# Kernel optimization log

Measured on AMD Instinct MI355X. Metric: run time of the kernel, lower is better.

The kernel has to match this reference:

```python
import jax, jax.numpy as jnp
import numpy as np

N, D_IN, HID, N_CLS, E = 100000, 256, 128, 41, 1600000


def setup_inputs() -> dict:
    key = jax.random.key(0)
    ks = jax.random.split(key, 8)
    x = jax.random.normal(ks[0], (N, D_IN), dtype=jnp.float32)
    edge_index = jax.random.randint(ks[1], (2, E), 0, N, dtype=jnp.int64)
    s = 1.0 / np.sqrt(D_IN)
    W1 = jax.random.uniform(ks[2], (D_IN, HID), jnp.float32, -s, s)
    b1 = jnp.zeros((HID,), jnp.float32)
    s2 = 1.0 / np.sqrt(HID)
    W2 = jax.random.uniform(ks[3], (HID, HID), jnp.float32, -s2, s2)
    b2 = jnp.zeros((HID,), jnp.float32)
    lin_w = jax.random.uniform(ks[4], (HID, N_CLS), jnp.float32, -s2, s2)
    lin_b = jnp.zeros((N_CLS,), jnp.float32)
    return {"x": x, "edge_index": edge_index, "W1": W1, "b1": b1,
            "W2": W2, "b2": b2, "lin_w": lin_w, "lin_b": lin_b}


def _gcn_conv(h, src, dst, norm, W, b, n):
    # h: [N, F_in]; transform then gather-scale-scatter (PyG GCNConv order)
    h = h @ W                                   # [N, F_out]
    msg = h[src] * norm[:, None]                # [E+N, F_out]
    return jax.ops.segment_sum(msg, dst, num_segments=n) + b


def reference(x, edge_index, W1, b1, W2, b2, lin_w, lin_b):
    n = x.shape[0]
    loops = jnp.arange(n, dtype=edge_index.dtype)
    src = jnp.concatenate([edge_index[0], loops])  # add self-loops
    dst = jnp.concatenate([edge_index[1], loops])
    # symmetric normalization D^-1/2 (A+I) D^-1/2
    deg = jax.ops.segment_sum(jnp.ones_like(dst, dtype=x.dtype), dst, num_segments=n)
    dis = jnp.where(deg > 0, jax.lax.rsqrt(jnp.maximum(deg, 1.0)), 0.0)
    norm = dis[src] * dis[dst]                   # [E+N]

    x1 = jax.nn.relu(_gcn_conv(x, src, dst, norm, W1, b1, n))   # dropout is identity in eval
    x2 = jax.nn.relu(_gcn_conv(x1, src, dst, norm, W2, b2, n))
    out = (x1 + x2) @ lin_w + lin_b
    return jax.nn.log_softmax(out, axis=1)
```

## Files before the change

kernel.cpp:

```cpp
#include <hip/hip_runtime.h>
#include <math.h>


#define NPAD (1 << 17)
#define CHUNK 1024

typedef __attribute__((ext_vector_type(8))) short short8;
typedef __attribute__((ext_vector_type(4))) float f32x4;

__device__ inline unsigned short f2bf(float f) {
    unsigned u = __builtin_bit_cast(unsigned, f);
    return (unsigned short)((u + 0x7fffu + ((u >> 16) & 1u)) >> 16);
}
__device__ inline float bflo(unsigned u) { return __builtin_bit_cast(float, u << 16); }
__device__ inline float bfhi(unsigned u) { return __builtin_bit_cast(float, u & 0xffff0000u); }


__global__ void mega1(const int* __restrict__ dst, int* __restrict__ cnt, int E, int histB,
                      const float* __restrict__ W1, unsigned short* __restrict__ Wt1,
                      const float* __restrict__ W2, unsigned short* __restrict__ Wt2) {
    int b = blockIdx.x;
    if (b < histB) {
        int e = b * 256 + threadIdx.x;
        if (e < E) atomicAdd(&cnt[dst[e]], 1);
    } else {
        int i = (b - histB) * 256 + threadIdx.x;
        if (i < 256 * 128) {
            int k = i >> 7, nn = i & 127;
            Wt1[nn * 256 + k] = f2bf(W1[i]);
        } else {
            int j = i - 256 * 128;
            if (j < 128 * 128) {
                int k = j >> 7, nn = j & 127;
                Wt2[nn * 128 + k] = f2bf(W2[j]);
            }
        }
    }
}

__global__ void scan_partial(const int* __restrict__ cnt, int* __restrict__ partial, int n) {
    __shared__ int sdata[4];
    int b = blockIdx.x, t = threadIdx.x;
    int base = b * CHUNK;
    int sum = 0;
    for (int i = t; i < CHUNK; i += 256) {
        int idx = base + i;
        if (idx < n) sum += cnt[idx];
    }
#pragma unroll
    for (int off = 32; off > 0; off >>= 1) sum += __shfl_down(sum, off, 64);
    if ((t & 63) == 0) sdata[t >> 6] = sum;
    __syncthreads();
    if (t == 0) partial[b] = sdata[0] + sdata[1] + sdata[2] + sdata[3];
}

__global__ void scan_small(int* partial, int nblk) {
    __shared__ int sm[128];
    int t = threadIdx.x;
    int v = (t < nblk) ? partial[t] : 0;
    int x = v;
    sm[t] = x;
    __syncthreads();
    for (int off = 1; off < 128; off <<= 1) {
        int y = (t >= off) ? sm[t - off] : 0;
        __syncthreads();
        x += y;
        sm[t] = x;
        __syncthreads();
    }
    if (t < nblk) partial[t] = x - v;
}

__global__ void scan_final(const int* __restrict__ cnt, const int* __restrict__ partial,
                           int* __restrict__ offs, int* __restrict__ cursor,
                           float* __restrict__ dis, int n) {
    __shared__ int wsum[4];
    int b = blockIdx.x, t = threadIdx.x;
    int lane = t & 63, w = t >> 6;
    int base = b * CHUNK + t * 4;
    int v[4];
#pragma unroll
    for (int j = 0; j < 4; j++) v[j] = (base + j < n) ? cnt[base + j] : 0;
    int s4 = v[0] + v[1] + v[2] + v[3];
    int inc = s4;
#pragma unroll
    for (int off = 1; off < 64; off <<= 1) {
        int x = __shfl_up(inc, off, 64);
        if (lane >= off) inc += x;
    }
    if (lane == 63) wsum[w] = inc;
    __syncthreads();
    int woff = 0;
    for (int i = 0; i < 4; i++) if (i < w) woff += wsum[i];
    int pos = partial[b] + woff + (inc - s4);
#pragma unroll
    for (int j = 0; j < 4; j++) {
        int idx = base + j;
        if (idx < n) {
            offs[idx] = pos;
            cursor[idx] = pos;
            dis[idx] = rsqrtf((float)(v[j] + 1));
            pos += v[j];
        }
    }
}

__global__ void permute_all(const int* __restrict__ src, const int* __restrict__ dst,
                            const float* __restrict__ dis,
                            int* __restrict__ cursor, int2* __restrict__ eadj, int E) {
    int e = blockIdx.x * 256 + threadIdx.x;
    if (e < E) {
        int d = dst[e];
        int s = src[e];
        int pos = atomicAdd(&cursor[d], 1);
        eadj[pos] = make_int2(s, __float_as_int(dis[s] * dis[d]));
    }
}

template<bool ABF16>
__device__ void gemm_body(int bid, const void* __restrict__ Ap,
                          const unsigned short* __restrict__ Wt,
                          unsigned short* __restrict__ Hb,
                          int n, int K, unsigned short* bs) {
    const int tid = threadIdx.x;
    const int wave = tid >> 6, lane = tid & 63;
    const int quad = lane >> 4, mrow = lane & 15;
    const int arow_g = bid * 64 + wave * 16 + mrow;
    const int arow = arow_g < n ? arow_g : n - 1;

    f32x4 acc[8];
#pragma unroll
    for (int t = 0; t < 8; t++) acc[t] = (f32x4){0.f, 0.f, 0.f, 0.f};

    const float* Af = (const float*)Ap;
    const unsigned short* Ab = (const unsigned short*)Ap;

    for (int kc = 0; kc < K; kc += 128) {
        __syncthreads();
        for (int i = tid; i < 2048; i += 256) {
            int row = i >> 4, c8 = i & 15;
            *(short8*)&bs[row * 136 + c8 * 8] = *(const short8*)&Wt[row * K + kc + c8 * 8];
        }
        __syncthreads();
#pragma unroll
        for (int kt = 0; kt < 128; kt += 32) {
            union { short8 v; unsigned short u[8]; } A;
            if (ABF16) {
                A.v = *(const short8*)&Ab[(size_t)arow * K + kc + kt + quad * 8];
            } else {
                const float* ap = &Af[(size_t)arow * K + kc + kt + quad * 8];
                float4 p0 = *(const float4*)ap;
                float4 p1 = *(const float4*)(ap + 4);
                A.u[0] = f2bf(p0.x); A.u[1] = f2bf(p0.y);
                A.u[2] = f2bf(p0.z); A.u[3] = f2bf(p0.w);
                A.u[4] = f2bf(p1.x); A.u[5] = f2bf(p1.y);
                A.u[6] = f2bf(p1.z); A.u[7] = f2bf(p1.w);
            }
#pragma unroll
            for (int nt = 0; nt < 8; nt++) {
                short8 B = *(const short8*)&bs[(nt * 16 + mrow) * 136 + kt + quad * 8];
                acc[nt] = __builtin_amdgcn_mfma_f32_16x16x32_bf16(A.v, B, acc[nt], 0, 0, 0);
            }
        }
    }
    const int drow0 = bid * 64 + wave * 16 + quad * 4;
#pragma unroll
    for (int r = 0; r < 4; r++) {
        int dr = drow0 + r;
        if (dr < n) {
#pragma unroll
            for (int nt = 0; nt < 8; nt++)
                Hb[(size_t)dr * 128 + nt * 16 + mrow] = f2bf(acc[nt][r]);
        }
    }
}

__global__ __launch_bounds__(256) void gemm1_k(const float* __restrict__ x,
                                               const unsigned short* __restrict__ Wt1,
                                               unsigned short* __restrict__ Hb, int n) {
    __shared__ unsigned short bs[128 * 136];
    gemm_body<false>(blockIdx.x, x, Wt1, Hb, n, 256, bs);
}

__global__ __launch_bounds__(256) void gemm2_k(const unsigned short* __restrict__ X1b,
                                               const unsigned short* __restrict__ Wt2,
                                               unsigned short* __restrict__ Hb, int n) {
    __shared__ unsigned short bs[128 * 136];
    gemm_body<true>(blockIdx.x, X1b, Wt2, Hb, n, 128, bs);
}

__global__ __launch_bounds__(256) void gather_h(const unsigned short* __restrict__ Hb,
                                                const int2* __restrict__ eadj,
                                                const int* __restrict__ offs,
                                                const int* __restrict__ cnt,
                                                const float* __restrict__ dis,
                                                const float* __restrict__ bias,
                                                unsigned short* __restrict__ outb,
                                                int n) {
    const int b = blockIdx.x;
    const int xcd = b & 7;
    const int half = xcd >> 2;
    const int nb = ((b >> 3) << 2) | (xcd & 3);
    const int w = threadIdx.x >> 6, lane = threadIdx.x & 63;
    const int grp = lane >> 3, fl = lane & 7;
    const int node = nb * 4 + w;
    const int nd = node < n ? node : n - 1;
    const int st = offs[nd], c = cnt[nd];
    const unsigned short* Hfl = Hb + half * 64 + fl * 8;

    float acc[8];
#pragma unroll
    for (int k = 0; k < 8; k++) acc[k] = 0.f;

    const int2* ep = eadj + st;
    for (int kk = 0; kk < c; kk += 64) {
        int li = kk + lane;
        int2 me = ep[li < c ? li : c - 1];
        float mw = li < c ? __int_as_float(me.y) : 0.f;
        int cend = (c - kk) < 64 ? (c - kk) : 64;

        int   s0 = __shfl(me.x, grp, 64);
        float w0 = __shfl(mw,  grp, 64);
        int   s1 = __shfl(me.x, 8 + grp, 64);
        float w1 = __shfl(mw,  8 + grp, 64);
        uint4 r0 = *(const uint4*)(Hfl + (size_t)s0 * 128);
        uint4 r1 = *(const uint4*)(Hfl + (size_t)s1 * 128);

        for (int j = 0; j < cend; j += 16) {
            int jn = (j + 16 < cend) ? j + 16 : j;
            int   sn0 = __shfl(me.x, jn + grp, 64);
            float wn0 = __shfl(mw,  jn + grp, 64);
            int   sn1 = __shfl(me.x, jn + 8 + grp, 64);
            float wn1 = __shfl(mw,  jn + 8 + grp, 64);
            uint4 rn0 = *(const uint4*)(Hfl + (size_t)sn0 * 128);
            uint4 rn1 = *(const uint4*)(Hfl + (size_t)sn1 * 128);
            acc[0] = fmaf(bflo(r0.x), w0, acc[0]); acc[1] = fmaf(bfhi(r0.x), w0, acc[1]);
            acc[2] = fmaf(bflo(r0.y), w0, acc[2]); acc[3] = fmaf(bfhi(r0.y), w0, acc[3]);
            acc[4] = fmaf(bflo(r0.z), w0, acc[4]); acc[5] = fmaf(bfhi(r0.z), w0, acc[5]);
            acc[6] = fmaf(bflo(r0.w), w0, acc[6]); acc[7] = fmaf(bfhi(r0.w), w0, acc[7]);
            acc[0] = fmaf(bflo(r1.x), w1, acc[0]); acc[1] = fmaf(bfhi(r1.x), w1, acc[1]);
            acc[2] = fmaf(bflo(r1.y), w1, acc[2]); acc[3] = fmaf(bfhi(r1.y), w1, acc[3]);
            acc[4] = fmaf(bflo(r1.z), w1, acc[4]); acc[5] = fmaf(bfhi(r1.z), w1, acc[5]);
            acc[6] = fmaf(bflo(r1.w), w1, acc[6]); acc[7] = fmaf(bfhi(r1.w), w1, acc[7]);
            r0 = rn0; r1 = rn1; w0 = wn0; w1 = wn1;
        }
    }
#pragma unroll
    for (int k = 0; k < 8; k++) {
        acc[k] += __shfl_xor(acc[k], 8, 64);
        acc[k] += __shfl_xor(acc[k], 16, 64);
        acc[k] += __shfl_xor(acc[k], 32, 64);
    }
    float dd = dis[nd], sn = dd * dd;
    uint4 rs = *(const uint4*)(Hfl + (size_t)nd * 128);
    float4 bb0 = ((const float4*)bias)[half * 16 + fl * 2];
    float4 bb1 = ((const float4*)bias)[half * 16 + fl * 2 + 1];
    acc[0] = fmaf(bflo(rs.x), sn, acc[0]) + bb0.x;
    acc[1] = fmaf(bfhi(rs.x), sn, acc[1]) + bb0.y;
    acc[2] = fmaf(bflo(rs.y), sn, acc[2]) + bb0.z;
    acc[3] = fmaf(bfhi(rs.y), sn, acc[3]) + bb0.w;
    acc[4] = fmaf(bflo(rs.z), sn, acc[4]) + bb1.x;
    acc[5] = fmaf(bfhi(rs.z), sn, acc[5]) + bb1.y;
    acc[6] = fmaf(bflo(rs.w), sn, acc[6]) + bb1.z;
    acc[7] = fmaf(bfhi(rs.w), sn, acc[7]) + bb1.w;
#pragma unroll
    for (int k = 0; k < 8; k++) acc[k] = acc[k] > 0.f ? acc[k] : 0.f;

    if (node < n && grp == 0) {
        uint4 pk;
        pk.x = ((unsigned)f2bf(acc[1]) << 16) | (unsigned)f2bf(acc[0]);
        pk.y = ((unsigned)f2bf(acc[3]) << 16) | (unsigned)f2bf(acc[2]);
        pk.z = ((unsigned)f2bf(acc[5]) << 16) | (unsigned)f2bf(acc[4]);
        pk.w = ((unsigned)f2bf(acc[7]) << 16) | (unsigned)f2bf(acc[6]);
        *(uint4*)(outb + (size_t)node * 128 + half * 64 + fl * 8) = pk;
    }
}

__global__ __launch_bounds__(256) void head_k(const unsigned short* __restrict__ x1b,
                                              const unsigned short* __restrict__ x2b,
                                              const float* __restrict__ lw,
                                              const float* __restrict__ lb,
                                              float* __restrict__ out, int n, int nblk) {
    __shared__ float lws[128 * 41];
    __shared__ float s[4][128];
    const int tid = threadIdx.x;
    const int w = tid >> 6, lane = tid & 63;
    for (int i = tid; i < 128 * 41; i += 256) lws[i] = lw[i];
    __syncthreads();
    const float lbv = (lane < 41) ? lb[lane] : 0.f;

    for (int blk = blockIdx.x; blk * 4 < n; blk += nblk) {
        const int node = blk * 4 + w;
        const int nd = node < n ? node : n - 1;
        unsigned u1 = *(const unsigned*)(x1b + (size_t)nd * 128 + lane * 2);
        unsigned u2 = *(const unsigned*)(x2b + (size_t)nd * 128 + lane * 2);
        s[w][lane * 2]     = bflo(u1) + bflo(u2);
        s[w][lane * 2 + 1] = bfhi(u1) + bfhi(u2);
        const bool act = (node < n) && (lane < 41);
        float v0 = 0.f, v1 = 0.f, v2 = 0.f, v3 = 0.f;
        if (act) {
#pragma unroll 8
            for (int f = 0; f < 32; f++) {
                v0 = fmaf(s[w][f],      lws[f * 41 + lane],        v0);
                v1 = fmaf(s[w][f + 32], lws[(f + 32) * 41 + lane], v1);
                v2 = fmaf(s[w][f + 64], lws[(f + 64) * 41 + lane], v2);
                v3 = fmaf(s[w][f + 96], lws[(f + 96) * 41 + lane], v3);
            }
        }
        float val = (v0 + v1) + (v2 + v3) + lbv;
        float m = act ? val : -INFINITY;
#pragma unroll
        for (int off = 32; off > 0; off >>= 1) m = fmaxf(m, __shfl_xor(m, off, 64));
        float e = act ? expf(val - m) : 0.f;
#pragma unroll
        for (int off = 32; off > 0; off >>= 1) e += __shfl_xor(e, off, 64);
        if (act) out[(size_t)node * 41 + lane] = val - m - logf(e);
    }
}

extern "C" void kernel_launch(void* const* d_in, const int* in_sizes, int n_in,
                              void* d_out, int out_size, void* d_ws, size_t ws_size,
                              hipStream_t stream) {
    const float* x  = (const float*)d_in[0];
    const int*   ei = (const int*)d_in[1];
    const float* W1 = (const float*)d_in[2];
    const float* b1 = (const float*)d_in[3];
    const float* W2 = (const float*)d_in[4];
    const float* b2 = (const float*)d_in[5];
    const float* lw = (const float*)d_in[6];
    const float* lb = (const float*)d_in[7];
    float* out = (float*)d_out;

    const int n = in_sizes[0] / 256;
    const int E = in_sizes[1] / 2;
    const int* src = ei;
    const int* dst = ei + E;

    int*   cnt     = (int*)d_ws;
    int*   offs    = cnt + NPAD;
    int*   cursor  = offs + NPAD;
    int*   partial = cursor + NPAD;
    float* dis     = (float*)(partial + 1024);
    size_t Epad    = ((size_t)E + 255) & ~(size_t)255;
    int2*  eadj    = (int2*)(dis + NPAD);
    unsigned short* Wt1 = (unsigned short*)(eadj + Epad);
    unsigned short* Wt2 = Wt1 + 256 * 128;
    unsigned short* Hb  = Wt2 + 128 * 128;
    unsigned short* X1b = Hb + (size_t)n * 128;
    unsigned short* X2b = X1b + (size_t)n * 128;

    const int nscan = (n + CHUNK - 1) / CHUNK;
    const int histB = (E + 255) / 256;
    const int wcastB = (256 * 128 + 128 * 128 + 255) / 256;
    const int gemmB = (n + 63) / 64;
    const int NB = (n + 3) / 4;
    const int gathB = 8 * ((NB + 3) / 4);
    const int headB = 1536;

    hipMemsetAsync(cnt, 0, (size_t)n * sizeof(int), stream);

    mega1<<<histB + wcastB, 256, 0, stream>>>(dst, cnt, E, histB, W1, Wt1, W2, Wt2);
    scan_partial<<<nscan, 256, 0, stream>>>(cnt, partial, n);
    scan_small<<<1, 128, 0, stream>>>(partial, nscan);
    scan_final<<<nscan, 256, 0, stream>>>(cnt, partial, offs, cursor, dis, n);
    permute_all<<<histB, 256, 0, stream>>>(src, dst, dis, cursor, eadj, E);

    gemm1_k<<<gemmB, 256, 0, stream>>>(x, Wt1, Hb, n);
    gather_h<<<gathB, 256, 0, stream>>>(Hb, eadj, offs, cnt, dis, b1, X1b, n);

    gemm2_k<<<gemmB, 256, 0, stream>>>(X1b, Wt2, Hb, n);
    gather_h<<<gathB, 256, 0, stream>>>(Hb, eadj, offs, cnt, dis, b2, X2b, n);

    head_k<<<headB, 256, 0, stream>>>(X1b, X2b, lw, lb, out, n, headB);
}
```

Before: 640.7 us.

## Compute classifier head with split-bf16 MFMA instead of scalar FMA loop

```diff
diff --git a/kernel.cpp b/kernel.cpp
--- a/kernel.cpp
+++ b/kernel.cpp
@@ -12,13 +12,18 @@
     unsigned u = __builtin_bit_cast(unsigned, f);
     return (unsigned short)((u + 0x7fffu + ((u >> 16) & 1u)) >> 16);
 }
+__device__ inline float bf2f(unsigned short h) {
+    return __builtin_bit_cast(float, (unsigned)h << 16);
+}
 __device__ inline float bflo(unsigned u) { return __builtin_bit_cast(float, u << 16); }
 __device__ inline float bfhi(unsigned u) { return __builtin_bit_cast(float, u & 0xffff0000u); }
 
 
 __global__ void mega1(const int* __restrict__ dst, int* __restrict__ cnt, int E, int histB,
                       const float* __restrict__ W1, unsigned short* __restrict__ Wt1,
-                      const float* __restrict__ W2, unsigned short* __restrict__ Wt2) {
+                      const float* __restrict__ W2, unsigned short* __restrict__ Wt2,
+                      const float* __restrict__ lw, unsigned short* __restrict__ lwt_hi,
+                      unsigned short* __restrict__ lwt_lo) {
     int b = blockIdx.x;
     if (b < histB) {
         int e = b * 256 + threadIdx.x;
@@ -28,11 +33,18 @@
         if (i < 256 * 128) {
             int k = i >> 7, nn = i & 127;
             Wt1[nn * 256 + k] = f2bf(W1[i]);
+        } else if (i < 256 * 128 + 128 * 128) {
+            int j = i - 256 * 128;
+            int k = j >> 7, nn = j & 127;
+            Wt2[nn * 128 + k] = f2bf(W2[j]);
         } else {
-            int j = i - 256 * 128;
-            if (j < 128 * 128) {
-                int k = j >> 7, nn = j & 127;
-                Wt2[nn * 128 + k] = f2bf(W2[j]);
+            int j = i - (256 * 128 + 128 * 128);
+            if (j < 48 * 128) {
+                int c = j >> 7, k = j & 127;
+                float wv = (c < 41) ? lw[k * 41 + c] : 0.f;
+                unsigned short hi = f2bf(wv);
+                lwt_hi[c * 128 + k] = hi;
+                lwt_lo[c * 128 + k] = f2bf(wv - bf2f(hi));
             }
         }
     }
@@ -278,43 +290,84 @@
 
 __global__ __launch_bounds__(256) void head_k(const unsigned short* __restrict__ x1b,
                                               const unsigned short* __restrict__ x2b,
-                                              const float* __restrict__ lw,
+                                              const unsigned short* __restrict__ lwt_hi,
+                                              const unsigned short* __restrict__ lwt_lo,
                                               const float* __restrict__ lb,
-                                              float* __restrict__ out, int n, int nblk) {
-    __shared__ float lws[128 * 41];
-    __shared__ float s[4][128];
+                                              float* __restrict__ out, int n) {
+    __shared__ unsigned short Ah[64][136];
+    __shared__ unsigned short Al[64][136];
+    __shared__ unsigned short Bh[48][136];
+    __shared__ unsigned short Bl[48][136];
     const int tid = threadIdx.x;
-    const int w = tid >> 6, lane = tid & 63;
-    for (int i = tid; i < 128 * 41; i += 256) lws[i] = lw[i];
+    const int wave = tid >> 6, lane = tid & 63;
+    const int quad = lane >> 4, mrow = lane & 15;
+    const int base = blockIdx.x * 64;
+
+    for (int i = tid; i < 1024; i += 256) {
+        int row = i >> 4, oct = i & 15;
+        int node = base + row; int nd = node < n ? node : n - 1;
+        uint4 u1 = *(const uint4*)(x1b + (size_t)nd * 128 + oct * 8);
+        uint4 u2 = *(const uint4*)(x2b + (size_t)nd * 128 + oct * 8);
+        unsigned uu1[4] = {u1.x, u1.y, u1.z, u1.w};
+        unsigned uu2[4] = {u2.x, u2.y, u2.z, u2.w};
+        union { short8 v; unsigned short u[8]; } H, L;
+#pragma unroll
+        for (int q = 0; q < 4; q++) {
+            float vl = bflo(uu1[q]) + bflo(uu2[q]);
+            float vh = bfhi(uu1[q]) + bfhi(uu2[q]);
+            unsigned short hl = f2bf(vl), hh = f2bf(vh);
+            H.u[q * 2]     = hl;  L.u[q * 2]     = f2bf(vl - bf2f(hl));
+            H.u[q * 2 + 1] = hh;  L.u[q * 2 + 1] = f2bf(vh - bf2f(hh));
+        }
+        *(short8*)&Ah[row][oct * 8] = H.v;
+        *(short8*)&Al[row][oct * 8] = L.v;
+    }
+    for (int i = tid; i < 768; i += 256) {
+        int row = i >> 4, oct = i & 15;
+        *(short8*)&Bh[row][oct * 8] = *(const short8*)&lwt_hi[row * 128 + oct * 8];
+        *(short8*)&Bl[row][oct * 8] = *(const short8*)&lwt_lo[row * 128 + oct * 8];
+    }
     __syncthreads();
-    const float lbv = (lane < 41) ? lb[lane] : 0.f;
-
-    for (int blk = blockIdx.x; blk * 4 < n; blk += nblk) {
-        const int node = blk * 4 + w;
-        const int nd = node < n ? node : n - 1;
-        unsigned u1 = *(const unsigned*)(x1b + (size_t)nd * 128 + lane * 2);
-        unsigned u2 = *(const unsigned*)(x2b + (size_t)nd * 128 + lane * 2);
-        s[w][lane * 2]     = bflo(u1) + bflo(u2);
-        s[w][lane * 2 + 1] = bfhi(u1) + bfhi(u2);
-        const bool act = (node < n) && (lane < 41);
-        float v0 = 0.f, v1 = 0.f, v2 = 0.f, v3 = 0.f;
-        if (act) {
-#pragma unroll 8
-            for (int f = 0; f < 32; f++) {
-                v0 = fmaf(s[w][f],      lws[f * 41 + lane],        v0);
-                v1 = fmaf(s[w][f + 32], lws[(f + 32) * 41 + lane], v1);
-                v2 = fmaf(s[w][f + 64], lws[(f + 64) * 41 + lane], v2);
-                v3 = fmaf(s[w][f + 96], lws[(f + 96) * 41 + lane], v3);
-            }
-        }
-        float val = (v0 + v1) + (v2 + v3) + lbv;
-        float m = act ? val : -INFINITY;
-#pragma unroll
-        for (int off = 32; off > 0; off >>= 1) m = fmaxf(m, __shfl_xor(m, off, 64));
-        float e = act ? expf(val - m) : 0.f;
-#pragma unroll
-        for (int off = 32; off > 0; off >>= 1) e += __shfl_xor(e, off, 64);
-        if (act) out[(size_t)node * 41 + lane] = val - m - logf(e);
+
+    f32x4 acc[3];
+#pragma unroll
+    for (int nt = 0; nt < 3; nt++) acc[nt] = (f32x4){0.f, 0.f, 0.f, 0.f};
+#pragma unroll
+    for (int kt = 0; kt < 128; kt += 32) {
+        short8 ah = *(short8*)&Ah[wave * 16 + mrow][kt + quad * 8];
+        short8 al = *(short8*)&Al[wave * 16 + mrow][kt + quad * 8];
+#pragma unroll
+        for (int nt = 0; nt < 3; nt++) {
+            short8 bh = *(short8*)&Bh[nt * 16 + mrow][kt + quad * 8];
+            short8 bl = *(short8*)&Bl[nt * 16 + mrow][kt + quad * 8];
+            acc[nt] = __builtin_amdgcn_mfma_f32_16x16x32_bf16(ah, bh, acc[nt], 0, 0, 0);
+            acc[nt] = __builtin_amdgcn_mfma_f32_16x16x32_bf16(ah, bl, acc[nt], 0, 0, 0);
+            acc[nt] = __builtin_amdgcn_mfma_f32_16x16x32_bf16(al, bh, acc[nt], 0, 0, 0);
+        }
+    }
+
+    const bool v2ok = (mrow < 9);
+    const float lb0 = lb[mrow];
+    const float lb1 = lb[16 + mrow];
+    const float lb2 = v2ok ? lb[32 + mrow] : 0.f;
+#pragma unroll
+    for (int r = 0; r < 4; r++) {
+        int node = base + wave * 16 + quad * 4 + r;
+        float v0 = acc[0][r] + lb0;
+        float v1 = acc[1][r] + lb1;
+        float v2 = v2ok ? acc[2][r] + lb2 : -INFINITY;
+        float m = fmaxf(fmaxf(v0, v1), v2);
+#pragma unroll
+        for (int off = 1; off < 16; off <<= 1) m = fmaxf(m, __shfl_xor(m, off, 64));
+        float e = expf(v0 - m) + expf(v1 - m) + (v2ok ? expf(v2 - m) : 0.f);
+#pragma unroll
+        for (int off = 1; off < 16; off <<= 1) e += __shfl_xor(e, off, 64);
+        float lse = m + logf(e);
+        if (node < n) {
+            out[(size_t)node * 41 + mrow] = v0 - lse;
+            out[(size_t)node * 41 + 16 + mrow] = v1 - lse;
+            if (v2ok) out[(size_t)node * 41 + 32 + mrow] = v2 - lse;
+        }
     }
 }
 
@@ -348,18 +401,20 @@
     unsigned short* Hb  = Wt2 + 128 * 128;
     unsigned short* X1b = Hb + (size_t)n * 128;
     unsigned short* X2b = X1b + (size_t)n * 128;
+    unsigned short* Lh  = X2b + (size_t)n * 128;
+    unsigned short* Ll  = Lh + 48 * 128;
 
     const int nscan = (n + CHUNK - 1) / CHUNK;
     const int histB = (E + 255) / 256;
-    const int wcastB = (256 * 128 + 128 * 128 + 255) / 256;
+    const int wcastB = (256 * 128 + 128 * 128 + 48 * 128 + 255) / 256;
     const int gemmB = (n + 63) / 64;
     const int NB = (n + 3) / 4;
     const int gathB = 8 * ((NB + 3) / 4);
-    const int headB = 1536;
 
     hipMemsetAsync(cnt, 0, (size_t)n * sizeof(int), stream);
 
-    mega1<<<histB + wcastB, 256, 0, stream>>>(dst, cnt, E, histB, W1, Wt1, W2, Wt2);
+    mega1<<<histB + wcastB, 256, 0, stream>>>(dst, cnt, E, histB, W1, Wt1, W2, Wt2,
+                                              lw, Lh, Ll);
     scan_partial<<<nscan, 256, 0, stream>>>(cnt, partial, n);
     scan_small<<<1, 128, 0, stream>>>(partial, nscan);
     scan_final<<<nscan, 256, 0, stream>>>(cnt, partial, offs, cursor, dis, n);
@@ -371,5 +426,5 @@
     gemm2_k<<<gemmB, 256, 0, stream>>>(X1b, Wt2, Hb, n);
     gather_h<<<gathB, 256, 0, stream>>>(Hb, eadj, offs, cnt, dis, b2, X2b, n);
 
-    head_k<<<headB, 256, 0, stream>>>(X1b, X2b, lw, lb, out, n, headB);
-}
+    head_k<<<gemmB, 256, 0, stream>>>(X1b, X2b, Lh, Ll, lb, out, n);
+}
```

Result: faster. 552.1 us (-13.8%).
